# Performance work log

Measured on AMD Instinct MI355X. Metric: run time of the kernel, lower is better.

The kernel has to match this reference:

```python
import jax, jax.numpy as jnp
import numpy as np

B, S, D = 2, 512, 64

def setup_inputs() -> dict:
    key = jax.random.key(0)
    k1, k2, k3, k4, k5 = jax.random.split(key, 5)
    x = jax.random.normal(k1, (B, S, D, D), dtype=jnp.float32)
    log_A = jax.random.normal(k2, (D,), dtype=jnp.float32) * 0.02
    # nn.Linear(dim, 1): weight (1, dim) -> store as (dim,), bias scalar
    dt_w = jax.random.normal(k3, (D,), dtype=jnp.float32) * (1.0 / np.sqrt(D))
    dt_b = jax.random.normal(k4, (), dtype=jnp.float32) * (1.0 / np.sqrt(D))
    # LayerNorm over normalized_shape=(dim, dim)
    ln_w = jnp.ones((D, D), dtype=jnp.float32)
    ln_b = jnp.zeros((D, D), dtype=jnp.float32)
    return {"x": x, "log_A": log_A, "dt_w": dt_w, "dt_b": dt_b, "ln_w": ln_w, "ln_b": ln_b}

def _layernorm_2d(x, w, b, eps=1e-5):
    # normalize over last two dims (d, d)
    mu = jnp.mean(x, axis=(-2, -1), keepdims=True)
    var = jnp.var(x, axis=(-2, -1), keepdims=True)
    return (x - mu) * jax.lax.rsqrt(var + eps) * w + b

def reference(x, log_A, dt_w, dt_b, ln_w, ln_b):
    b, seq, d, _ = x.shape
    x_in = x
    xn = _layernorm_2d(x, ln_w, ln_b)                      # (b, s, d, d)
    A_cont = -jnp.exp(log_A)                               # (d,)
    dt = jax.nn.softplus(jnp.einsum('bsdc,c->bsd', xn, dt_w) + dt_b)  # (b, s, d)
    log_A_dt = dt * A_cont                                 # (b, s, d)
    cs = jnp.cumsum(log_A_dt, axis=1)                      # (b, s, d)
    log_M = cs[:, :, None, :] - cs[:, None, :, :]          # (b, t, j, d)
    idx = jnp.arange(seq)
    mask = (idx[:, None] >= idx[None, :])[None, :, :, None]  # causal (1, t, j, 1)
    M = jnp.exp(jnp.where(mask, log_M, -jnp.inf))          # (b, t, j, d)
    out = jnp.einsum('btjr,bjrc->btrc', M, xn)             # (b, t, d, d)
    return out + x_in
```

## Files before the change

kernel.cpp:

```cpp
#include <hip/hip_runtime.h>
#include <math.h>

#define BB 2
#define SS 512
#define DD 64
#define DDDD 4096
#define NC 16
#define CL (SS / NC)

__global__ __launch_bounds__(256) void k1_stats(
    const float* __restrict__ x, const float* __restrict__ log_A,
    const float* __restrict__ dt_w, const float* __restrict__ dt_b,
    const float* __restrict__ ln_w, const float* __restrict__ ln_b,
    float* __restrict__ a_out, float2* __restrict__ stats)
{
    const int bs  = blockIdx.x;
    const int tid = threadIdx.x;

    const float4* xp4 = (const float4*)(x + (size_t)bs * DDDD + tid * 16);
    float4 v0 = xp4[0], v1 = xp4[1], v2 = xp4[2], v3 = xp4[3];

    float sum = (v0.x+v0.y+v0.z+v0.w) + (v1.x+v1.y+v1.z+v1.w)
              + (v2.x+v2.y+v2.z+v2.w) + (v3.x+v3.y+v3.z+v3.w);
    float sq  = (v0.x*v0.x+v0.y*v0.y+v0.z*v0.z+v0.w*v0.w)
              + (v1.x*v1.x+v1.y*v1.y+v1.z*v1.z+v1.w*v1.w)
              + (v2.x*v2.x+v2.y*v2.y+v2.z*v2.z+v2.w*v2.w)
              + (v3.x*v3.x+v3.y*v3.y+v3.z*v3.z+v3.w*v3.w);

    #pragma unroll
    for (int off = 32; off > 0; off >>= 1) {
        sum += __shfl_down(sum, off);
        sq  += __shfl_down(sq,  off);
    }
    __shared__ float s_sum[4], s_sq[4];
    const int wv = tid >> 6, ln = tid & 63;
    if (ln == 0) { s_sum[wv] = sum; s_sq[wv] = sq; }
    __syncthreads();
    const float tsum = s_sum[0] + s_sum[1] + s_sum[2] + s_sum[3];
    const float tsq  = s_sq[0]  + s_sq[1]  + s_sq[2]  + s_sq[3];
    const float mu   = tsum * (1.0f / DDDD);
    const float var  = tsq  * (1.0f / DDDD) - mu * mu;
    const float rstd = rsqrtf(var + 1e-5f);

    const float4* lw4 = (const float4*)(ln_w + tid * 16);
    const float4* lb4 = (const float4*)(ln_b + tid * 16);
    const float4* dw4 = (const float4*)(dt_w + (tid & 3) * 16);
    float p = 0.f;
    #define ACC4(vv, ii) { \
        float4 lw = lw4[ii], lb = lb4[ii], dw = dw4[ii];            \
        p = fmaf(fmaf((vv.x - mu) * rstd, lw.x, lb.x), dw.x, p);    \
        p = fmaf(fmaf((vv.y - mu) * rstd, lw.y, lb.y), dw.y, p);    \
        p = fmaf(fmaf((vv.z - mu) * rstd, lw.z, lb.z), dw.z, p);    \
        p = fmaf(fmaf((vv.w - mu) * rstd, lw.w, lb.w), dw.w, p);    \
    }
    ACC4(v0, 0); ACC4(v1, 1); ACC4(v2, 2); ACC4(v3, 3);
    #undef ACC4

    p += __shfl_xor(p, 1);
    p += __shfl_xor(p, 2);

    if ((tid & 3) == 0) {
        const int d = tid >> 2;
        float z = p + dt_b[0];
        float dt = (z > 20.f) ? z : log1pf(expf(z));
        float la = dt * (-expf(log_A[d]));
        a_out[bs * DD + d] = expf(la);
    }
    if (tid == 0) stats[bs] = make_float2(mu, rstd);
}

__global__ __launch_bounds__(256) void k2a_partial(
    const float* __restrict__ x, const float* __restrict__ a_in,
    const float* __restrict__ ln_w, const float* __restrict__ ln_b,
    const float2* __restrict__ stats,
    float* __restrict__ Fbuf, float* __restrict__ Pbuf)
{
    const int gw = blockIdx.x * 4 + (threadIdx.x >> 6);
    const int c  = threadIdx.x & 63;
    const int ch = gw & (NC - 1);
    const int br = gw >> 4;
    const int b  = br >> 6, r = br & 63;

    const float lnw = ln_w[r * DD + c];
    const float lnb = ln_b[r * DD + c];

    const int t0 = ch * CL;
    const float*  xp = x + (((size_t)(b * SS + t0)) * DD + r) * DD + c;
    const float*  ap = a_in + (b * SS + t0) * DD + r;
    const float2* sp = stats + b * SS + t0;

    float state = 0.f, P = 1.f;
    for (int t = 0; t < CL; t += 8) {
        float xv[8], av[8]; float2 st[8];
        #pragma unroll
        for (int i = 0; i < 8; ++i) {
            xv[i] = xp[(size_t)(t + i) * DDDD];
            av[i] = ap[(t + i) * DD];
            st[i] = sp[t + i];
        }
        #pragma unroll
        for (int i = 0; i < 8; ++i) {
            float xn = fmaf((xv[i] - st[i].x) * st[i].y, lnw, lnb);
            state = fmaf(av[i], state, xn);
            P *= av[i];
        }
    }
    Fbuf[(size_t)gw * DD + c] = state;
    if (c == 0) Pbuf[gw] = P;
}

__global__ __launch_bounds__(256) void k2b_final(
    const float* __restrict__ x, const float* __restrict__ a_in,
    const float* __restrict__ ln_w, const float* __restrict__ ln_b,
    const float2* __restrict__ stats,
    const float* __restrict__ Fbuf, const float* __restrict__ Pbuf,
    float* __restrict__ out)
{
    const int gw = blockIdx.x * 4 + (threadIdx.x >> 6);
    const int c  = threadIdx.x & 63;
    const int ch = gw & (NC - 1);
    const int br = gw >> 4;
    const int b  = br >> 6, r = br & 63;

    float f[NC], p[NC];
    #pragma unroll
    for (int v = 0; v < NC; ++v) {
        f[v] = Fbuf[(size_t)(br * NC + v) * DD + c];
        p[v] = Pbuf[br * NC + v];
    }
    float carry = 0.f;
    #pragma unroll
    for (int v = 0; v < NC; ++v) {
        float pv = (v < ch) ? p[v] : 1.f;
        float fv = (v < ch) ? f[v] : 0.f;
        carry = fmaf(pv, carry, fv);
    }

    const float lnw = ln_w[r * DD + c];
    const float lnb = ln_b[r * DD + c];

    const int t0 = ch * CL;
    const size_t xoff = (((size_t)(b * SS + t0)) * DD + r) * DD + c;
    const float*  xp = x + xoff;
    const float*  ap = a_in + (b * SS + t0) * DD + r;
    const float2* sp = stats + b * SS + t0;
    float* op = out + xoff;

    float state = carry;
    for (int t = 0; t < CL; t += 8) {
        float xv[8], av[8]; float2 st[8];
        #pragma unroll
        for (int i = 0; i < 8; ++i) {
            xv[i] = xp[(size_t)(t + i) * DDDD];
            av[i] = ap[(t + i) * DD];
            st[i] = sp[t + i];
        }
        #pragma unroll
        for (int i = 0; i < 8; ++i) {
            float xn = fmaf((xv[i] - st[i].x) * st[i].y, lnw, lnb);
            state = fmaf(av[i], state, xn);
            op[(size_t)(t + i) * DDDD] = state + xv[i];
        }
    }
}

extern "C" void kernel_launch(void* const* d_in, const int* in_sizes, int n_in,
                              void* d_out, int out_size, void* d_ws, size_t ws_size,
                              hipStream_t stream) {
    const float* x     = (const float*)d_in[0];
    const float* log_A = (const float*)d_in[1];
    const float* dt_w  = (const float*)d_in[2];
    const float* dt_b  = (const float*)d_in[3];
    const float* ln_w  = (const float*)d_in[4];
    const float* ln_b  = (const float*)d_in[5];
    float* out = (float*)d_out;

    char* ws = (char*)d_ws;
    float*  a_buf = (float*)ws;
    float2* stats = (float2*)(ws + 262144);
    float*  Fbuf  = (float*)(ws + 262144 + 8192);
    float*  Pbuf  = (float*)(ws + 262144 + 8192 + 524288);

    k1_stats<<<BB * SS, 256, 0, stream>>>(x, log_A, dt_w, dt_b, ln_w, ln_b, a_buf, stats);
    k2a_partial<<<BB * DD * NC / 4, 256, 0, stream>>>(x, a_buf, ln_w, ln_b, stats, Fbuf, Pbuf);
    k2b_final<<<BB * DD * NC / 4, 256, 0, stream>>>(x, a_buf, ln_w, ln_b, stats, Fbuf, Pbuf, out);
}
```

Baseline: 89.88 us.

## Fuse three phases into one cooperative kernel with grid syncs

Merges the stats, chunk-partial scan and final scan kernels into a single cooperative kernel with two grid-wide barriers, so two launch gaps disappear. It restructures the dt projection algebraically: the raw dot with ln_w*dt_w is taken in phase A, and the mean/rstd correction is applied later inside the scan phase. It also doubles the chunk count to 32 with 16 steps each, giving more parallel work per scan. The cost is grid-sync overhead and needing all 1024 blocks co-resident; if the cooperative launch fails it falls back to three separate kernels.

New measurement: 309.3 us. 244% more time.

```diff
diff --git a/kernel.cpp b/kernel.cpp
--- a/kernel.cpp
+++ b/kernel.cpp
@@ -1,167 +1,192 @@
 #include <hip/hip_runtime.h>
+#include <hip/hip_cooperative_groups.h>
 #include <math.h>
+
+namespace cg = cooperative_groups;
 
 #define BB 2
 #define SS 512
 #define DD 64
-#define DDDD 4096
-#define NC 16
-#define CL (SS / NC)
-
-__global__ __launch_bounds__(256) void k1_stats(
+#define NC 32
+#define CL 16
+
+__device__ __forceinline__ void phaseA_body(
+    const float* __restrict__ x, const float* __restrict__ ln_w,
+    const float* __restrict__ dt_w,
+    float2* __restrict__ partA, float* __restrict__ zbuf,
+    int gwA, int ln)
+{
+    const int bt = gwA >> 2;
+    const int q  = gwA & 3;
+    const float4* xp = (const float4*)(x + (size_t)bt * 4096 + q * 1024 + ln * 16);
+    const float4* wp = (const float4*)(ln_w + q * 1024 + ln * 16);
+    const float4* dp = (const float4*)(dt_w + (ln & 3) * 16);
+
+    float s1 = 0.f, s2 = 0.f, z = 0.f;
+    #pragma unroll
+    for (int i = 0; i < 4; ++i) {
+        float4 v = xp[i], w = wp[i], dv = dp[i];
+        s1 += v.x + v.y + v.z + v.w;
+        s2 += v.x*v.x + v.y*v.y + v.z*v.z + v.w*v.w;
+        z  += v.x*w.x*dv.x + v.y*w.y*dv.y + v.z*w.z*dv.z + v.w*w.w*dv.w;
+    }
+    #pragma unroll
+    for (int off = 32; off; off >>= 1) {
+        s1 += __shfl_xor(s1, off);
+        s2 += __shfl_xor(s2, off);
+    }
+    z += __shfl_xor(z, 1);
+    z += __shfl_xor(z, 2);
+    if (ln == 0) partA[gwA] = make_float2(s1, s2);
+    if ((ln & 3) == 0) zbuf[bt * DD + (q * 16 + (ln >> 2))] = z;
+}
+
+__device__ __forceinline__ void phaseB_body(
+    const float* __restrict__ x, const float* __restrict__ log_A,
+    const float* __restrict__ dt_b, const float* __restrict__ ln_w,
+    const float* __restrict__ ln_b, const float* __restrict__ dt_w,
+    const float2* __restrict__ partA, const float* __restrict__ zbuf,
+    float2* __restrict__ statbuf, float* __restrict__ abuf,
+    float* __restrict__ Fbuf, float* __restrict__ Pbuf,
+    int gw, int c)
+{
+    const int ch = gw & (NC - 1);
+    const int br = gw >> 5;
+    const int b  = br >> 6, r = br & 63;
+    const int t0 = ch * CL;
+
+    const float lnw = ln_w[r * DD + c];
+    const float lnb = ln_b[r * DD + c];
+    const float dwc = dt_w[c];
+    float w1 = lnw * dwc, b1 = lnb * dwc;
+    #pragma unroll
+    for (int off = 32; off; off >>= 1) {
+        w1 += __shfl_xor(w1, off);
+        b1 += __shfl_xor(b1, off);
+    }
+    const float Ar  = -expf(log_A[r]);
+    const float dtb = dt_b[0];
+
+    const size_t xbase = (((size_t)(b * SS + t0)) * DD + r) * DD + c;
+    float state = 0.f, P = 1.f;
+    #pragma unroll 4
+    for (int t = 0; t < CL; ++t) {
+        const int bt = b * SS + t0 + t;
+        const float4* pa = (const float4*)(partA + bt * 4);
+        float4 A0 = pa[0], A1 = pa[1];
+        const float s1 = A0.x + A0.z + A1.x + A1.z;
+        const float s2 = A0.y + A0.w + A1.y + A1.w;
+        const float mu   = s1 * (1.0f / 4096.0f);
+        const float var  = s2 * (1.0f / 4096.0f) - mu * mu;
+        const float rstd = rsqrtf(var + 1e-5f);
+        const float zr = zbuf[bt * DD + r];
+        const float zz = fmaf(rstd, zr - mu * w1, b1) + dtb;
+        const float dt = (zz > 20.f) ? zz : log1pf(expf(zz));
+        const float av = expf(dt * Ar);
+        const float xv = x[xbase + (size_t)t * DD * DD];
+        const float xn = fmaf((xv - mu) * rstd, lnw, lnb);
+        state = fmaf(av, state, xn);
+        P *= av;
+        if (c == 0) abuf[bt * DD + r] = av;
+        if (c == 0 && r == 0) statbuf[bt] = make_float2(mu, rstd);
+    }
+    Fbuf[(size_t)gw * DD + c] = state;
+    if (c == 0) Pbuf[gw] = P;
+}
+
+__device__ __forceinline__ void phaseC_body(
+    const float* __restrict__ x, const float* __restrict__ ln_w,
+    const float* __restrict__ ln_b,
+    const float2* __restrict__ statbuf, const float* __restrict__ abuf,
+    const float* __restrict__ Fbuf, const float* __restrict__ Pbuf,
+    float* __restrict__ out, int gw, int c)
+{
+    const int ch = gw & (NC - 1);
+    const int br = gw >> 5;
+    const int b  = br >> 6, r = br & 63;
+    const int t0 = ch * CL;
+    const float lnw = ln_w[r * DD + c];
+    const float lnb = ln_b[r * DD + c];
+
+    float carry = 0.f;
+    for (int vb = 0; vb < NC; vb += 8) {
+        float f[8], p[8];
+        #pragma unroll
+        for (int i = 0; i < 8; ++i) {
+            f[i] = Fbuf[(size_t)(br * NC + vb + i) * DD + c];
+            p[i] = Pbuf[br * NC + vb + i];
+        }
+        #pragma unroll
+        for (int i = 0; i < 8; ++i) {
+            const int v = vb + i;
+            carry = fmaf((v < ch) ? p[i] : 1.f, carry, (v < ch) ? f[i] : 0.f);
+        }
+    }
+
+    const size_t xbase = (((size_t)(b * SS + t0)) * DD + r) * DD + c;
+    float st = carry;
+    #pragma unroll 4
+    for (int t = 0; t < CL; ++t) {
+        const int bt = b * SS + t0 + t;
+        const float2 ms = statbuf[bt];
+        const float av = abuf[bt * DD + r];
+        const float xv = x[xbase + (size_t)t * DD * DD];
+        const float xn = fmaf((xv - ms.x) * ms.y, lnw, lnb);
+        st = fmaf(av, st, xn);
+        out[xbase + (size_t)t * DD * DD] = st + xv;
+    }
+}
+
+__global__ __launch_bounds__(256) void fused_all(
     const float* __restrict__ x, const float* __restrict__ log_A,
     const float* __restrict__ dt_w, const float* __restrict__ dt_b,
     const float* __restrict__ ln_w, const float* __restrict__ ln_b,
-    float* __restrict__ a_out, float2* __restrict__ stats)
-{
-    const int bs  = blockIdx.x;
-    const int tid = threadIdx.x;
-
-    const float4* xp4 = (const float4*)(x + (size_t)bs * DDDD + tid * 16);
-    float4 v0 = xp4[0], v1 = xp4[1], v2 = xp4[2], v3 = xp4[3];
-
-    float sum = (v0.x+v0.y+v0.z+v0.w) + (v1.x+v1.y+v1.z+v1.w)
-              + (v2.x+v2.y+v2.z+v2.w) + (v3.x+v3.y+v3.z+v3.w);
-    float sq  = (v0.x*v0.x+v0.y*v0.y+v0.z*v0.z+v0.w*v0.w)
-              + (v1.x*v1.x+v1.y*v1.y+v1.z*v1.z+v1.w*v1.w)
-              + (v2.x*v2.x+v2.y*v2.y+v2.z*v2.z+v2.w*v2.w)
-              + (v3.x*v3.x+v3.y*v3.y+v3.z*v3.z+v3.w*v3.w);
-
-    #pragma unroll
-    for (int off = 32; off > 0; off >>= 1) {
-        sum += __shfl_down(sum, off);
-        sq  += __shfl_down(sq,  off);
-    }
-    __shared__ float s_sum[4], s_sq[4];
-    const int wv = tid >> 6, ln = tid & 63;
-    if (ln == 0) { s_sum[wv] = sum; s_sq[wv] = sq; }
-    __syncthreads();
-    const float tsum = s_sum[0] + s_sum[1] + s_sum[2] + s_sum[3];
-    const float tsq  = s_sq[0]  + s_sq[1]  + s_sq[2]  + s_sq[3];
-    const float mu   = tsum * (1.0f / DDDD);
-    const float var  = tsq  * (1.0f / DDDD) - mu * mu;
-    const float rstd = rsqrtf(var + 1e-5f);
-
-    const float4* lw4 = (const float4*)(ln_w + tid * 16);
-    const float4* lb4 = (const float4*)(ln_b + tid * 16);
-    const float4* dw4 = (const float4*)(dt_w + (tid & 3) * 16);
-    float p = 0.f;
-    #define ACC4(vv, ii) { \
-        float4 lw = lw4[ii], lb = lb4[ii], dw = dw4[ii];            \
-        p = fmaf(fmaf((vv.x - mu) * rstd, lw.x, lb.x), dw.x, p);    \
-        p = fmaf(fmaf((vv.y - mu) * rstd, lw.y, lb.y), dw.y, p);    \
-        p = fmaf(fmaf((vv.z - mu) * rstd, lw.z, lb.z), dw.z, p);    \
-        p = fmaf(fmaf((vv.w - mu) * rstd, lw.w, lb.w), dw.w, p);    \
-    }
-    ACC4(v0, 0); ACC4(v1, 1); ACC4(v2, 2); ACC4(v3, 3);
-    #undef ACC4
-
-    p += __shfl_xor(p, 1);
-    p += __shfl_xor(p, 2);
-
-    if ((tid & 3) == 0) {
-        const int d = tid >> 2;
-        float z = p + dt_b[0];
-        float dt = (z > 20.f) ? z : log1pf(expf(z));
-        float la = dt * (-expf(log_A[d]));
-        a_out[bs * DD + d] = expf(la);
-    }
-    if (tid == 0) stats[bs] = make_float2(mu, rstd);
-}
-
-__global__ __launch_bounds__(256) void k2a_partial(
-    const float* __restrict__ x, const float* __restrict__ a_in,
-    const float* __restrict__ ln_w, const float* __restrict__ ln_b,
-    const float2* __restrict__ stats,
+    float* __restrict__ out,
+    float2* __restrict__ partA, float* __restrict__ zbuf,
+    float2* __restrict__ statbuf, float* __restrict__ abuf,
     float* __restrict__ Fbuf, float* __restrict__ Pbuf)
 {
-    const int gw = blockIdx.x * 4 + (threadIdx.x >> 6);
-    const int c  = threadIdx.x & 63;
-    const int ch = gw & (NC - 1);
-    const int br = gw >> 4;
-    const int b  = br >> 6, r = br & 63;
-
-    const float lnw = ln_w[r * DD + c];
-    const float lnb = ln_b[r * DD + c];
-
-    const int t0 = ch * CL;
-    const float*  xp = x + (((size_t)(b * SS + t0)) * DD + r) * DD + c;
-    const float*  ap = a_in + (b * SS + t0) * DD + r;
-    const float2* sp = stats + b * SS + t0;
-
-    float state = 0.f, P = 1.f;
-    for (int t = 0; t < CL; t += 8) {
-        float xv[8], av[8]; float2 st[8];
-        #pragma unroll
-        for (int i = 0; i < 8; ++i) {
-            xv[i] = xp[(size_t)(t + i) * DDDD];
-            av[i] = ap[(t + i) * DD];
-            st[i] = sp[t + i];
-        }
-        #pragma unroll
-        for (int i = 0; i < 8; ++i) {
-            float xn = fmaf((xv[i] - st[i].x) * st[i].y, lnw, lnb);
-            state = fmaf(av[i], state, xn);
-            P *= av[i];
-        }
-    }
-    Fbuf[(size_t)gw * DD + c] = state;
-    if (c == 0) Pbuf[gw] = P;
-}
-
-__global__ __launch_bounds__(256) void k2b_final(
-    const float* __restrict__ x, const float* __restrict__ a_in,
-    const float* __restrict__ ln_w, const float* __restrict__ ln_b,
-    const float2* __restrict__ stats,
+    const int wv = threadIdx.x >> 6, ln = threadIdx.x & 63;
+    const int gw = blockIdx.x * 4 + wv;
+    phaseA_body(x, ln_w, dt_w, partA, zbuf, gw, ln);
+    cg::this_grid().sync();
+    phaseB_body(x, log_A, dt_b, ln_w, ln_b, dt_w, partA, zbuf,
+                statbuf, abuf, Fbuf, Pbuf, gw, ln);
+    cg::this_grid().sync();
+    phaseC_body(x, ln_w, ln_b, statbuf, abuf, Fbuf, Pbuf, out, gw, ln);
+}
+
+__global__ __launch_bounds__(256) void kA(
+    const float* __restrict__ x, const float* __restrict__ ln_w,
+    const float* __restrict__ dt_w,
+    float2* __restrict__ partA, float* __restrict__ zbuf)
+{
+    phaseA_body(x, ln_w, dt_w, partA, zbuf,
+                blockIdx.x * 4 + (threadIdx.x >> 6), threadIdx.x & 63);
+}
+
+__global__ __launch_bounds__(256) void kB(
+    const float* __restrict__ x, const float* __restrict__ log_A,
+    const float* __restrict__ dt_b, const float* __restrict__ ln_w,
+    const float* __restrict__ ln_b, const float* __restrict__ dt_w,
+    const float2* __restrict__ partA, const float* __restrict__ zbuf,
+    float2* __restrict__ statbuf, float* __restrict__ abuf,
+    float* __restrict__ Fbuf, float* __restrict__ Pbuf)
+{
+    phaseB_body(x, log_A, dt_b, ln_w, ln_b, dt_w, partA, zbuf,
+                statbuf, abuf, Fbuf, Pbuf,
+                blockIdx.x * 4 + (threadIdx.x >> 6), threadIdx.x & 63);
+}
+
+__global__ __launch_bounds__(256) void kC(
+    const float* __restrict__ x, const float* __restrict__ ln_w,
+    const float* __restrict__ ln_b,
+    const float2* __restrict__ statbuf, const float* __restrict__ abuf,
     const float* __restrict__ Fbuf, const float* __restrict__ Pbuf,
     float* __restrict__ out)
 {
-    const int gw = blockIdx.x * 4 + (threadIdx.x >> 6);
-    const int c  = threadIdx.x & 63;
-    const int ch = gw & (NC - 1);
-    const int br = gw >> 4;
-    const int b  = br >> 6, r = br & 63;
-
-    float f[NC], p[NC];
-    #pragma unroll
-    for (int v = 0; v < NC; ++v) {
-        f[v] = Fbuf[(size_t)(br * NC + v) * DD + c];
-        p[v] = Pbuf[br * NC + v];
-    }
-    float carry = 0.f;
-    #pragma unroll
-    for (int v = 0; v < NC; ++v) {
-        float pv = (v < ch) ? p[v] : 1.f;
-        float fv = (v < ch) ? f[v] : 0.f;
-        carry = fmaf(pv, carry, fv);
-    }
-
-    const float lnw = ln_w[r * DD + c];
-    const float lnb = ln_b[r * DD + c];
-
-    const int t0 = ch * CL;
-    const size_t xoff = (((size_t)(b * SS + t0)) * DD + r) * DD + c;
-    const float*  xp = x + xoff;
-    const float*  ap = a_in + (b * SS + t0) * DD + r;
-    const float2* sp = stats + b * SS + t0;
-    float* op = out + xoff;
-
-    float state = carry;
-    for (int t = 0; t < CL; t += 8) {
-        float xv[8], av[8]; float2 st[8];
-        #pragma unroll
-        for (int i = 0; i < 8; ++i) {
-            xv[i] = xp[(size_t)(t + i) * DDDD];
-            av[i] = ap[(t + i) * DD];
-            st[i] = sp[t + i];
-        }
-        #pragma unroll
-        for (int i = 0; i < 8; ++i) {
-            float xn = fmaf((xv[i] - st[i].x) * st[i].y, lnw, lnb);
-            state = fmaf(av[i], state, xn);
-            op[(size_t)(t + i) * DDDD] = state + xv[i];
-        }
-    }
+    phaseC_body(x, ln_w, ln_b, statbuf, abuf, Fbuf, Pbuf, out,
+                blockIdx.x * 4 + (threadIdx.x >> 6), threadIdx.x & 63);
 }
 
 extern "C" void kernel_launch(void* const* d_in, const int* in_sizes, int n_in,
@@ -176,12 +201,27 @@
     float* out = (float*)d_out;
 
     char* ws = (char*)d_ws;
-    float*  a_buf = (float*)ws;
-    float2* stats = (float2*)(ws + 262144);
-    float*  Fbuf  = (float*)(ws + 262144 + 8192);
-    float*  Pbuf  = (float*)(ws + 262144 + 8192 + 524288);
-
-    k1_stats<<<BB * SS, 256, 0, stream>>>(x, log_A, dt_w, dt_b, ln_w, ln_b, a_buf, stats);
-    k2a_partial<<<BB * DD * NC / 4, 256, 0, stream>>>(x, a_buf, ln_w, ln_b, stats, Fbuf, Pbuf);
-    k2b_final<<<BB * DD * NC / 4, 256, 0, stream>>>(x, a_buf, ln_w, ln_b, stats, Fbuf, Pbuf, out);
-}
+    float2* partA   = (float2*)(ws);
+    float*  zbuf    = (float*)(ws + (64 << 10));
+    float2* statbuf = (float2*)(ws + (320 << 10));
+    float*  abuf    = (float*)(ws + (384 << 10));
+    float*  Fbuf    = (float*)(ws + (640 << 10));
+    float*  Pbuf    = (float*)(ws + (1664 << 10));
+
+    void* args[] = {
+        (void*)&x, (void*)&log_A, (void*)&dt_w, (void*)&dt_b,
+        (void*)&ln_w, (void*)&ln_b, (void*)&out,
+        (void*)&partA, (void*)&zbuf, (void*)&statbuf, (void*)&abuf,
+        (void*)&Fbuf, (void*)&Pbuf
+    };
+    hipError_t err = hipLaunchCooperativeKernel((const void*)fused_all,
+                                                dim3(BB * SS * 4 / 4), dim3(256),
+                                                args, 0, stream);
+    if (err != hipSuccess) {
+        kA<<<BB * SS, 256, 0, stream>>>(x, ln_w, dt_w, partA, zbuf);
+        kB<<<BB * DD * NC / 4, 256, 0, stream>>>(x, log_A, dt_b, ln_w, ln_b, dt_w,
+                                                 partA, zbuf, statbuf, abuf, Fbuf, Pbuf);
+        kC<<<BB * DD * NC / 4, 256, 0, stream>>>(x, ln_w, ln_b, statbuf, abuf,
+                                                 Fbuf, Pbuf, out);
+    }
+}
```

## Use float4 per-lane scan with 64 time chunks and remapped wave layout

Applied to the files above, without the earlier changes.

The chunked scan now splits the sequence into 64 chunks of 8 steps instead of 16 chunks of 32. Each lane handles four contiguous columns through float4 loads and stores, and each wave covers four rows of one chunk. The goal is more parallel work per launch, shorter serial dependency chains, and wider memory transactions. In exchange, the carry-combine pass in the final kernel reads more chunk partials per row (64 instead of 16), and the partial buffers grow.

New measurement: 96.59 us. 7.5% more time.

```diff
diff --git a/kernel.cpp b/kernel.cpp
--- a/kernel.cpp
+++ b/kernel.cpp
@@ -5,7 +5,7 @@
 #define SS 512
 #define DD 64
 #define DDDD 4096
-#define NC 16
+#define NC 64
 #define CL (SS / NC)
 
 __global__ __launch_bounds__(256) void k1_stats(
@@ -69,44 +69,44 @@
     if (tid == 0) stats[bs] = make_float2(mu, rstd);
 }
 
+
 __global__ __launch_bounds__(256) void k2a_partial(
     const float* __restrict__ x, const float* __restrict__ a_in,
     const float* __restrict__ ln_w, const float* __restrict__ ln_b,
     const float2* __restrict__ stats,
     float* __restrict__ Fbuf, float* __restrict__ Pbuf)
 {
-    const int gw = blockIdx.x * 4 + (threadIdx.x >> 6);
-    const int c  = threadIdx.x & 63;
-    const int ch = gw & (NC - 1);
-    const int br = gw >> 4;
-    const int b  = br >> 6, r = br & 63;
+    const int gw   = blockIdx.x * 4 + (threadIdx.x >> 6);
+    const int lane = threadIdx.x & 63;
+    const int b  = gw >> 10;
+    const int ch = (gw >> 4) & (NC - 1);
+    const int rg = gw & 15;
+    const int r  = rg * 4 + (lane >> 4);
+    const int c4 = (lane & 15) * 4;
+    const int t0 = ch * CL;
 
-    const float lnw = ln_w[r * DD + c];
-    const float lnb = ln_b[r * DD + c];
+    const float4 lnw4 = *(const float4*)(ln_w + r * DD + c4);
+    const float4 lnb4 = *(const float4*)(ln_b + r * DD + c4);
 
-    const int t0 = ch * CL;
-    const float*  xp = x + (((size_t)(b * SS + t0)) * DD + r) * DD + c;
+    const float*  xp = x + (((size_t)(b * SS + t0)) * DD + r) * DD + c4;
     const float*  ap = a_in + (b * SS + t0) * DD + r;
     const float2* sp = stats + b * SS + t0;
 
-    float state = 0.f, P = 1.f;
-    for (int t = 0; t < CL; t += 8) {
-        float xv[8], av[8]; float2 st[8];
-        #pragma unroll
-        for (int i = 0; i < 8; ++i) {
-            xv[i] = xp[(size_t)(t + i) * DDDD];
-            av[i] = ap[(t + i) * DD];
-            st[i] = sp[t + i];
-        }
-        #pragma unroll
-        for (int i = 0; i < 8; ++i) {
-            float xn = fmaf((xv[i] - st[i].x) * st[i].y, lnw, lnb);
-            state = fmaf(av[i], state, xn);
-            P *= av[i];
-        }
+    float4 st = make_float4(0.f, 0.f, 0.f, 0.f);
+    float  P  = 1.f;
+    #pragma unroll
+    for (int t = 0; t < CL; ++t) {
+        const float4 xv = *(const float4*)(xp + (size_t)t * DDDD);
+        const float  av = ap[t * DD];
+        const float2 ms = sp[t];
+        st.x = fmaf(av, st.x, fmaf((xv.x - ms.x) * ms.y, lnw4.x, lnb4.x));
+        st.y = fmaf(av, st.y, fmaf((xv.y - ms.x) * ms.y, lnw4.y, lnb4.y));
+        st.z = fmaf(av, st.z, fmaf((xv.z - ms.x) * ms.y, lnw4.z, lnb4.z));
+        st.w = fmaf(av, st.w, fmaf((xv.w - ms.x) * ms.y, lnw4.w, lnb4.w));
+        P *= av;
     }
-    Fbuf[(size_t)gw * DD + c] = state;
-    if (c == 0) Pbuf[gw] = P;
+    *(float4*)(Fbuf + (((size_t)(b * DD + r)) * NC + ch) * DD + c4) = st;
+    if ((lane & 15) == 0) Pbuf[(b * DD + r) * NC + ch] = P;
 }
 
 __global__ __launch_bounds__(256) void k2b_final(
@@ -116,51 +116,60 @@
     const float* __restrict__ Fbuf, const float* __restrict__ Pbuf,
     float* __restrict__ out)
 {
-    const int gw = blockIdx.x * 4 + (threadIdx.x >> 6);
-    const int c  = threadIdx.x & 63;
-    const int ch = gw & (NC - 1);
-    const int br = gw >> 4;
-    const int b  = br >> 6, r = br & 63;
+    const int gw   = blockIdx.x * 4 + (threadIdx.x >> 6);
+    const int lane = threadIdx.x & 63;
+    const int b  = gw >> 10;
+    const int ch = (gw >> 4) & (NC - 1);
+    const int rg = gw & 15;
+    const int r  = rg * 4 + (lane >> 4);
+    const int c4 = (lane & 15) * 4;
+    const int t0 = ch * CL;
 
-    float f[NC], p[NC];
-    #pragma unroll
-    for (int v = 0; v < NC; ++v) {
-        f[v] = Fbuf[(size_t)(br * NC + v) * DD + c];
-        p[v] = Pbuf[br * NC + v];
-    }
-    float carry = 0.f;
-    #pragma unroll
-    for (int v = 0; v < NC; ++v) {
-        float pv = (v < ch) ? p[v] : 1.f;
-        float fv = (v < ch) ? f[v] : 0.f;
-        carry = fmaf(pv, carry, fv);
+    const float* fb = Fbuf + ((size_t)(b * DD + r)) * NC * DD + c4;
+    const float* pb = Pbuf + (b * DD + r) * NC;
+    float4 carry = make_float4(0.f, 0.f, 0.f, 0.f);
+    for (int vb = 0; vb < NC; vb += 8) {
+        float4 f[8]; float p[8];
+        #pragma unroll
+        for (int i = 0; i < 8; ++i) {
+            f[i] = *(const float4*)(fb + (size_t)(vb + i) * DD);
+            p[i] = pb[vb + i];
+        }
+        #pragma unroll
+        for (int i = 0; i < 8; ++i) {
+            const int v = vb + i;
+            const bool pre = (v < ch);
+            const float pv = pre ? p[i] : 1.f;
+            carry.x = fmaf(pv, carry.x, pre ? f[i].x : 0.f);
+            carry.y = fmaf(pv, carry.y, pre ? f[i].y : 0.f);
+            carry.z = fmaf(pv, carry.z, pre ? f[i].z : 0.f);
+            carry.w = fmaf(pv, carry.w, pre ? f[i].w : 0.f);
+        }
     }
 
-    const float lnw = ln_w[r * DD + c];
-    const float lnb = ln_b[r * DD + c];
+    const float4 lnw4 = *(const float4*)(ln_w + r * DD + c4);
+    const float4 lnb4 = *(const float4*)(ln_b + r * DD + c4);
 
-    const int t0 = ch * CL;
-    const size_t xoff = (((size_t)(b * SS + t0)) * DD + r) * DD + c;
+    const size_t xoff = (((size_t)(b * SS + t0)) * DD + r) * DD + c4;
     const float*  xp = x + xoff;
     const float*  ap = a_in + (b * SS + t0) * DD + r;
     const float2* sp = stats + b * SS + t0;
     float* op = out + xoff;
 
-    float state = carry;
-    for (int t = 0; t < CL; t += 8) {
-        float xv[8], av[8]; float2 st[8];
-        #pragma unroll
-        for (int i = 0; i < 8; ++i) {
-            xv[i] = xp[(size_t)(t + i) * DDDD];
-            av[i] = ap[(t + i) * DD];
-            st[i] = sp[t + i];
-        }
-        #pragma unroll
-        for (int i = 0; i < 8; ++i) {
-            float xn = fmaf((xv[i] - st[i].x) * st[i].y, lnw, lnb);
-            state = fmaf(av[i], state, xn);
-            op[(size_t)(t + i) * DDDD] = state + xv[i];
-        }
+    float4 st = carry;
+    #pragma unroll
+    for (int t = 0; t < CL; ++t) {
+        const float4 xv = *(const float4*)(xp + (size_t)t * DDDD);
+        const float  av = ap[t * DD];
+        const float2 ms = sp[t];
+        st.x = fmaf(av, st.x, fmaf((xv.x - ms.x) * ms.y, lnw4.x, lnb4.x));
+        st.y = fmaf(av, st.y, fmaf((xv.y - ms.x) * ms.y, lnw4.y, lnb4.y));
+        st.z = fmaf(av, st.z, fmaf((xv.z - ms.x) * ms.y, lnw4.z, lnb4.z));
+        st.w = fmaf(av, st.w, fmaf((xv.w - ms.x) * ms.y, lnw4.w, lnb4.w));
+        float4 o;
+        o.x = st.x + xv.x; o.y = st.y + xv.y;
+        o.z = st.z + xv.z; o.w = st.w + xv.w;
+        *(float4*)(op + (size_t)t * DDDD) = o;
     }
 }
 
@@ -177,11 +186,11 @@
 
     char* ws = (char*)d_ws;
     float*  a_buf = (float*)ws;
-    float2* stats = (float2*)(ws + 262144);
-    float*  Fbuf  = (float*)(ws + 262144 + 8192);
-    float*  Pbuf  = (float*)(ws + 262144 + 8192 + 524288);
+    float2* stats = (float2*)(ws + (256 << 10));
+    float*  Fbuf  = (float*)(ws + (264 << 10));
+    float*  Pbuf  = (float*)(ws + (264 << 10) + (2 << 20));
 
     k1_stats<<<BB * SS, 256, 0, stream>>>(x, log_A, dt_w, dt_b, ln_w, ln_b, a_buf, stats);
-    k2a_partial<<<BB * DD * NC / 4, 256, 0, stream>>>(x, a_buf, ln_w, ln_b, stats, Fbuf, Pbuf);
-    k2b_final<<<BB * DD * NC / 4, 256, 0, stream>>>(x, a_buf, ln_w, ln_b, stats, Fbuf, Pbuf, out);
+    k2a_partial<<<BB * NC * 16 / 4, 256, 0, stream>>>(x, a_buf, ln_w, ln_b, stats, Fbuf, Pbuf);
+    k2b_final<<<BB * NC * 16 / 4, 256, 0, stream>>>(x, a_buf, ln_w, ln_b, stats, Fbuf, Pbuf, out);
 }
```
